# Kernel optimization log

Measured on AMD Instinct MI355X. Metric: run time of the kernel, lower is better.

Reference implementation:

```python
import jax, jax.numpy as jnp
import numpy as np

D = 2048
N = 16384
E = 8
THRESHOLD = 0.5


def setup_inputs() -> dict:
    key = jax.random.key(0)
    ks = jax.random.split(key, 6)
    x = jax.random.normal(ks[0], (N, D), dtype=jnp.float32)
    # pretrained weight + truncated SVD basis (frozen in original module)
    W_np = np.asarray(jax.random.normal(ks[1], (D, D), dtype=jnp.float32))
    U, S, Vt = np.linalg.svd(W_np, full_matrices=False)
    k = int((np.cumsum(S) < THRESHOLD * S.sum()).sum())  # energy-threshold rank
    U_k = jnp.asarray(U[:, :k])
    V_k = jnp.asarray(Vt.T[:, :k])  # torch.svd returns V, not V^T
    W = jnp.asarray(W_np)
    lambda_k = jax.random.normal(ks[2], (E, k), dtype=jnp.float32)
    v = jnp.zeros((D,), dtype=jnp.float32)
    W_g1 = jax.random.normal(ks[3], (k, 1), dtype=jnp.float32)
    W_g2 = jax.random.normal(ks[4], (1, E), dtype=jnp.float32)
    return {"x": x, "W": W, "U_k": U_k, "V_k": V_k, "lambda_k": lambda_k,
            "v": v, "W_g1": W_g1, "W_g2": W_g2}


def reference(x, W, U_k, V_k, lambda_k, v, W_g1, W_g2):
    # Routing: g = softmax((x @ U_k) @ W_g1 @ W_g2)  -> [N, E]
    xu = x @ U_k                                   # [N, k] (shared with delta path)
    g = jax.nn.softmax((xu @ W_g1) @ W_g2, axis=-1)
    # sum_i g_i * (x @ (W + U diag(lam_i) V^T))
    #   = (x@W) * sum_i g_i  +  ((x@U) * (g @ lam)) @ V^T   (low-rank factored)
    base = x @ W                                   # [N, D], computed once
    coef = g @ lambda_k                            # [N, k]
    out = base * jnp.sum(g, axis=-1, keepdims=True) + (xu * coef) @ V_k.T
    return out * (1.0 + v)
```

## Files before the change

kernel.cpp:

```cpp
#include <hip/hip_runtime.h>
#include <hip/hip_bf16.h>

#define D_DIM 2048
#define E_DIM 8

typedef __attribute__((ext_vector_type(8))) short short8;
typedef __attribute__((ext_vector_type(4))) float f32x4;

__device__ __forceinline__ unsigned short f2bf(float f) {
  union { float f; unsigned int u; } v; v.f = f;
  unsigned int u = v.u;
  u += 0x7FFFu + ((u >> 16) & 1u);
  return (unsigned short)(u >> 16);
}

__device__ __forceinline__ float bf2f(unsigned short h) {
  union { unsigned int u; float f; } v; v.u = ((unsigned int)h) << 16;
  return v.f;
}

__device__ __forceinline__ void async_copy16(const void* g, void* l) {
  __builtin_amdgcn_global_load_lds((const __attribute__((address_space(1))) void*)g,
                                   (__attribute__((address_space(3))) void*)l,
                                   16, 0, 0);
}

__global__ void k_cvt_bf16(const float* __restrict__ in,
                           unsigned short* __restrict__ out, long long n) {
  long long i = ((long long)blockIdx.x * blockDim.x + threadIdx.x) * 8;
  const long long stride = (long long)gridDim.x * blockDim.x * 8;
  for (; i < n; i += stride) {
    float4 a = *(const float4*)(in + i);
    float4 b = *(const float4*)(in + i + 4);
    short8 r;
    r[0] = (short)f2bf(a.x); r[1] = (short)f2bf(a.y);
    r[2] = (short)f2bf(a.z); r[3] = (short)f2bf(a.w);
    r[4] = (short)f2bf(b.x); r[5] = (short)f2bf(b.y);
    r[6] = (short)f2bf(b.z); r[7] = (short)f2bf(b.w);
    *(short8*)(out + i) = r;
  }
}

__global__ void k_transpose_bf16(const float* __restrict__ in, int in_rows, int in_cols,
                                 int in_ld, unsigned short* __restrict__ out, int out_rows) {
  __shared__ float tile[32][33];
  const int tx = threadIdx.x;
  const int ty = threadIdx.y;
  const int c = blockIdx.x * 32 + tx;
  #pragma unroll
  for (int i = 0; i < 4; ++i) {
    const int r = blockIdx.y * 32 + ty + i * 8;
    float vv = 0.0f;
    if (r < in_rows && c < in_cols) vv = in[(size_t)r * in_ld + c];
    tile[ty + i * 8][tx] = vv;
  }
  __syncthreads();
  const int oc = blockIdx.y * 32 + tx;
  #pragma unroll
  for (int i = 0; i < 4; ++i) {
    const int orow = blockIdx.x * 32 + ty + i * 8;
    if (orow < out_rows && oc < in_rows)
      out[(size_t)orow * in_rows + oc] = f2bf(tile[tx][ty + i * 8]);
  }
}

__global__ void k_pad_bf16(const float* __restrict__ in, unsigned short* __restrict__ out,
                           int rows, int cols, int cols_pad) {
  long long idx = (long long)blockIdx.x * blockDim.x + threadIdx.x;
  const long long total = (long long)rows * cols_pad;
  const long long stride = (long long)gridDim.x * blockDim.x;
  for (; idx < total; idx += stride) {
    const int r = (int)(idx / cols_pad);
    const int c = (int)(idx % cols_pad);
    out[idx] = (c < cols) ? f2bf(in[(size_t)r * cols + c]) : (unsigned short)0;
  }
}

__global__ void k_u1(const float* __restrict__ U, const float* __restrict__ Wg1,
                     float* __restrict__ u1, int D, int k) {
  const int w = threadIdx.x >> 6;
  const int lane = threadIdx.x & 63;
  const int d = blockIdx.x * 4 + w;
  if (d >= D) return;
  const float* row = U + (size_t)d * k;
  float s = 0.0f;
  for (int j = lane; j < k; j += 64) s += row[j] * Wg1[j];
  #pragma unroll
  for (int off = 32; off; off >>= 1) s += __shfl_xor(s, off);
  if (lane == 0) u1[d] = s;
}

__global__ void k_gate(const unsigned short* __restrict__ xb,
                       const float* __restrict__ u1, const float* __restrict__ Wg2,
                       float* __restrict__ g8, int Nrows) {
  const int w = threadIdx.x >> 6;
  const int lane = threadIdx.x & 63;
  const int row = blockIdx.x * 4 + w;
  if (row >= Nrows) return;
  const unsigned short* xr = xb + (size_t)row * D_DIM;
  float s = 0.0f;
  #pragma unroll
  for (int t = 0; t < D_DIM / 512; ++t) {
    const int base = (t * 64 + lane) * 8;
    short8 v = *(const short8*)(xr + base);
    float4 ua = *(const float4*)(u1 + base);
    float4 ub = *(const float4*)(u1 + base + 4);
    s += bf2f((unsigned short)v[0]) * ua.x + bf2f((unsigned short)v[1]) * ua.y +
         bf2f((unsigned short)v[2]) * ua.z + bf2f((unsigned short)v[3]) * ua.w +
         bf2f((unsigned short)v[4]) * ub.x + bf2f((unsigned short)v[5]) * ub.y +
         bf2f((unsigned short)v[6]) * ub.z + bf2f((unsigned short)v[7]) * ub.w;
  }
  #pragma unroll
  for (int off = 32; off; off >>= 1) s += __shfl_xor(s, off);
  if (lane == 0) {
    float lg[E_DIM], mx = -INFINITY;
    #pragma unroll
    for (int e = 0; e < E_DIM; ++e) { lg[e] = s * Wg2[e]; mx = fmaxf(mx, lg[e]); }
    float Z = 0.0f;
    #pragma unroll
    for (int e = 0; e < E_DIM; ++e) { lg[e] = expf(lg[e] - mx); Z += lg[e]; }
    const float inv = 1.0f / Z;
    #pragma unroll
    for (int e = 0; e < E_DIM; ++e) g8[(size_t)row * E_DIM + e] = lg[e] * inv;
  }
}

__global__ __launch_bounds__(256, 3) void k_gemm128(
    const unsigned short* __restrict__ A, long long lda,
    const unsigned short* __restrict__ B, long long ldb,
    int Ktot,
    const float* __restrict__ g8, const float* __restrict__ lam, int k_real,
    unsigned short* __restrict__ A2, int lda2) {
  __shared__ unsigned short lds[2 * 8192];
  const int tid = threadIdx.x;
  const int lane = tid & 63;
  const int w = tid >> 6;
  const long long brow = (long long)blockIdx.x * 128;
  const long long bcol = (long long)blockIdx.y * 128;
  const int c0 = w * 2;
  const int sr0 = lane >> 2;
  const int sj  = lane & 3;
  const int l15 = lane & 15;
  const int jhi = lane >> 4;
  const int wr = (w >> 1) * 64;
  const int wc = (w & 1) * 64;

  auto stage = [&](int tt) {
    unsigned short* dstA = lds + (tt & 1) * 8192;
    #pragma unroll
    for (int c = 0; c < 2; ++c) {
      const int chunk = c0 + c;
      const int lrow = chunk * 16 + sr0;
      const int jj = sj ^ ((lrow >> 1) & 3);
      async_copy16(A + (brow + lrow) * lda + (long long)tt * 32 + jj * 8,
                   (void*)(dstA + chunk * 512));
      async_copy16(B + (bcol + lrow) * ldb + (long long)tt * 32 + jj * 8,
                   (void*)(dstA + 4096 + chunk * 512));
    }
  };

  f32x4 acc[4][4];
  #pragma unroll
  for (int m = 0; m < 4; ++m)
    #pragma unroll
    for (int n = 0; n < 4; ++n)
      #pragma unroll
      for (int j = 0; j < 4; ++j) acc[m][n][j] = 0.0f;

  const int NT = Ktot >> 5;
  stage(0);
  asm volatile("s_waitcnt vmcnt(0)" ::: "memory");
  __builtin_amdgcn_s_barrier();

  for (int t = 0; t < NT; ++t) {
    const unsigned short* Areg = lds + (t & 1) * 8192;
    const unsigned short* Breg = Areg + 4096;
    if (t + 1 < NT) stage(t + 1);
    short8 av[4], bv[4];
    #pragma unroll
    for (int m = 0; m < 4; ++m) {
      const int row = wr + m * 16 + l15;
      const int jj = jhi ^ ((row >> 1) & 3);
      av[m] = *(const short8*)(Areg + row * 32 + jj * 8);
    }
    #pragma unroll
    for (int n = 0; n < 4; ++n) {
      const int row = wc + n * 16 + l15;
      const int jj = jhi ^ ((row >> 1) & 3);
      bv[n] = *(const short8*)(Breg + row * 32 + jj * 8);
    }
    __builtin_amdgcn_s_setprio(1);
    #pragma unroll
    for (int m = 0; m < 4; ++m)
      #pragma unroll
      for (int n = 0; n < 4; ++n)
        acc[m][n] = __builtin_amdgcn_mfma_f32_16x16x32_bf16(av[m], bv[n], acc[m][n], 0, 0, 0);
    __builtin_amdgcn_s_setprio(0);
    asm volatile("s_waitcnt vmcnt(0)" ::: "memory");
    __builtin_amdgcn_s_barrier();
  }

  float lamE[E_DIM][4];
  #pragma unroll
  for (int n = 0; n < 4; ++n) {
    const long long col = bcol + wc + n * 16 + l15;
    #pragma unroll
    for (int e = 0; e < E_DIM; ++e)
      lamE[e][n] = (col < k_real) ? lam[(size_t)e * k_real + col] : 0.0f;
  }
  #pragma unroll
  for (int m = 0; m < 4; ++m) {
    float coef[4][4];
    #pragma unroll
    for (int j = 0; j < 4; ++j)
      #pragma unroll
      for (int n = 0; n < 4; ++n) coef[j][n] = 0.0f;
    #pragma unroll
    for (int j = 0; j < 4; ++j) {
      const long long row = brow + wr + m * 16 + jhi * 4 + j;
      const float* gr = g8 + row * E_DIM;
      #pragma unroll
      for (int e = 0; e < E_DIM; ++e) {
        const float ge = gr[e];
        #pragma unroll
        for (int n = 0; n < 4; ++n) coef[j][n] += ge * lamE[e][n];
      }
    }
    #pragma unroll
    for (int n = 0; n < 4; ++n) {
      const long long col = bcol + wc + n * 16 + l15;
      #pragma unroll
      for (int j = 0; j < 4; ++j) {
        const long long row = brow + wr + m * 16 + jhi * 4 + j;
        A2[row * lda2 + col] = f2bf(acc[m][n][j] * coef[j][n]);
      }
    }
  }
}

template<int EPI>
__global__ __launch_bounds__(512, 2) void k_gemm256(
    const unsigned short* __restrict__ A0, int lda0,
    const unsigned short* __restrict__ A1, int lda1,
    const unsigned short* __restrict__ B0, int ldb0,
    const unsigned short* __restrict__ B1, int ldb1,
    int ka0, int Ktot, int gridM,
    float* __restrict__ Cout, int ldc,
    const float* __restrict__ vcol) {
  __shared__ unsigned short lds[4 * 16384];
  const int tid = threadIdx.x;
  const int lane = tid & 63;
  const int w = tid >> 6;
  const int wm = w >> 2;
  const int wn = w & 3;

  int bid = blockIdx.x;
  const int cpx = gridDim.x >> 3;
  bid = (bid & 7) * cpx + (bid >> 3);
  const int bx = bid % gridM;
  const int by = bid / gridM;
  const long long brow = (long long)bx * 256;
  const long long bcol = (long long)by * 256;

  const int c0 = w * 2;
  const int sr0 = lane >> 2;
  const int sj  = lane & 3;
  const int l15 = lane & 15;
  const int jhi = lane >> 4;

  auto stage = [&](int tt) {
    const int k0 = tt * 32;
    const unsigned short* PA; long long ldA; long long kA;
    const unsigned short* PB; long long ldB; long long kB;
    if (k0 < ka0) { PA = A0; ldA = lda0; kA = k0;       PB = B0; ldB = ldb0; kB = k0; }
    else          { PA = A1; ldA = lda1; kA = k0 - ka0; PB = B1; ldB = ldb1; kB = k0 - ka0; }
    unsigned short* dst = lds + (tt & 3) * 16384;
    #pragma unroll
    for (int c = 0; c < 2; ++c) {
      const int chunk = c0 + c;
      const int lrow = chunk * 16 + sr0;
      const int jj = sj ^ ((lrow >> 1) & 3);
      async_copy16(PA + (brow + lrow) * ldA + kA + jj * 8, (void*)(dst + chunk * 512));
      async_copy16(PB + (bcol + lrow) * ldB + kB + jj * 8, (void*)(dst + 8192 + chunk * 512));
    }
  };

  auto load_frags = [&](int tt, short8* av, short8* bv) {
    const unsigned short* Areg = lds + (tt & 3) * 16384;
    const unsigned short* Breg = Areg + 8192;
    #pragma unroll
    for (int m = 0; m < 8; ++m) {
      const int row = wm * 128 + m * 16 + l15;
      const int jj = jhi ^ ((row >> 1) & 3);
      av[m] = *(const short8*)(Areg + row * 32 + jj * 8);
    }
    #pragma unroll
    for (int n = 0; n < 4; ++n) {
      const int row = wn * 64 + n * 16 + l15;
      const int jj = jhi ^ ((row >> 1) & 3);
      bv[n] = *(const short8*)(Breg + row * 32 + jj * 8);
    }
  };

  f32x4 acc[8][4];
  #pragma unroll
  for (int m = 0; m < 8; ++m)
    #pragma unroll
    for (int n = 0; n < 4; ++n)
      #pragma unroll
      for (int j = 0; j < 4; ++j) acc[m][n][j] = 0.0f;

  auto do_mfma = [&](short8* av, short8* bv) {
    __builtin_amdgcn_s_setprio(1);
    #pragma unroll
    for (int m = 0; m < 8; ++m)
      #pragma unroll
      for (int n = 0; n < 4; ++n)
        acc[m][n] = __builtin_amdgcn_mfma_f32_16x16x32_bf16(av[m], bv[n], acc[m][n], 0, 0, 0);
    __builtin_amdgcn_s_setprio(0);
  };

  const int NT = Ktot >> 5;
  stage(0); stage(1); stage(2);
  asm volatile("s_waitcnt vmcnt(4)" ::: "memory");
  __builtin_amdgcn_s_barrier();

  short8 avA[8], bvA[4], avB[8], bvB[4];
  load_frags(0, avA, bvA);

  for (int t = 0; t < NT; t += 2) {
    if (t + 3 < NT) stage(t + 3);
    load_frags(t + 1, avB, bvB);
    do_mfma(avA, bvA);
    asm volatile("s_waitcnt vmcnt(4)" ::: "memory");
    __builtin_amdgcn_s_barrier();
    if (t + 4 < NT) stage(t + 4);
    if (t + 2 < NT) load_frags(t + 2, avA, bvA);
    do_mfma(avB, bvB);
    asm volatile("s_waitcnt vmcnt(4)" ::: "memory");
    __builtin_amdgcn_s_barrier();
  }

  #pragma unroll
  for (int m = 0; m < 8; ++m) {
    #pragma unroll
    for (int n = 0; n < 4; ++n) {
      const long long col = bcol + wn * 64 + n * 16 + l15;
      float cs = 1.0f;
      if (EPI == 1) cs = 1.0f + vcol[col];
      #pragma unroll
      for (int j = 0; j < 4; ++j) {
        const long long row = brow + wm * 128 + m * 16 + jhi * 4 + j;
        Cout[row * ldc + col] = acc[m][n][j] * cs;
      }
    }
  }
}

extern "C" void kernel_launch(void* const* d_in, const int* in_sizes, int n_in,
                              void* d_out, int out_size, void* d_ws, size_t ws_size,
                              hipStream_t stream) {
  const float* x   = (const float*)d_in[0];
  const float* W   = (const float*)d_in[1];
  const float* U   = (const float*)d_in[2];
  const float* V   = (const float*)d_in[3];
  const float* lam = (const float*)d_in[4];
  const float* v   = (const float*)d_in[5];
  const float* Wg1 = (const float*)d_in[6];
  const float* Wg2 = (const float*)d_in[7];
  float* out = (float*)d_out;

  const int N = in_sizes[0] / D_DIM;
  const int k = in_sizes[2] / D_DIM;
  const int k_pad = (k + 127) & ~127;

  char* ws = (char*)d_ws;
  size_t off = 0;
  auto alloc = [&](size_t bytes) -> void* {
    void* p = ws + off;
    off += (bytes + 255) & ~(size_t)255;
    return p;
  };
  unsigned short* xb  = (unsigned short*)alloc((size_t)N * D_DIM * 2);
  unsigned short* Wt  = (unsigned short*)alloc((size_t)D_DIM * D_DIM * 2);
  unsigned short* Ukt = (unsigned short*)alloc((size_t)k_pad * D_DIM * 2);
  unsigned short* Vb  = (unsigned short*)alloc((size_t)D_DIM * k_pad * 2);
  unsigned short* A2  = (unsigned short*)alloc((size_t)N * k_pad * 2);
  float*          u1  = (float*)alloc((size_t)D_DIM * 4);
  float*          g8  = (float*)alloc((size_t)N * E_DIM * 4);
  if (off > ws_size) return;

  k_cvt_bf16<<<2048, 256, 0, stream>>>(x, xb, (long long)N * D_DIM);
  k_transpose_bf16<<<dim3(D_DIM / 32, D_DIM / 32), dim3(32, 8), 0, stream>>>(
      W, D_DIM, D_DIM, D_DIM, Wt, D_DIM);
  k_transpose_bf16<<<dim3(k_pad / 32, D_DIM / 32), dim3(32, 8), 0, stream>>>(
      U, D_DIM, k, k, Ukt, k_pad);
  k_pad_bf16<<<512, 256, 0, stream>>>(V, Vb, D_DIM, k, k_pad);
  k_u1<<<D_DIM / 4, 256, 0, stream>>>(U, Wg1, u1, D_DIM, k);

  k_gate<<<N / 4, 256, 0, stream>>>(xb, u1, Wg2, g8, N);

  k_gemm128<<<dim3(N / 128, k_pad / 128), 256, 0, stream>>>(
      xb, D_DIM, Ukt, D_DIM, D_DIM, g8, lam, k, A2, k_pad);

  const int gridM = N / 256;
  const int gridN = D_DIM / 256;
  k_gemm256<1><<<gridM * gridN, 512, 0, stream>>>(
      xb, D_DIM, A2, k_pad,
      Wt, D_DIM, Vb, k_pad,
      D_DIM, D_DIM + k_pad, gridM,
      out, D_DIM, v);
}
```

Baseline: 327.8 us.

## Fuse x bf16 conversion into gate kernel and switch main GEMM to 32x32 MFMA

Merges the standalone fp32-to-bf16 conversion of x into the gating kernel, so x is read once in fp32 and the gate dot product uses full-precision values while the bf16 copy is written. This drops one full read of the bf16 x buffer and a kernel launch. The large 256-tile GEMM now uses 32x32x16 bf16 MFMA instead of 16x16x32, with fragment loads and the epilogue row mapping rewritten to match. That cuts the number of MFMA issues and LDS fragment reads per tile, but the epilogue store pattern changes.

```diff
diff --git a/kernel.cpp b/kernel.cpp
--- a/kernel.cpp
+++ b/kernel.cpp
@@ -6,6 +6,7 @@
 
 typedef __attribute__((ext_vector_type(8))) short short8;
 typedef __attribute__((ext_vector_type(4))) float f32x4;
+typedef __attribute__((ext_vector_type(16))) float f32x16;
 
 __device__ __forceinline__ unsigned short f2bf(float f) {
   union { float f; unsigned int u; } v; v.f = f;
@@ -14,31 +15,10 @@
   return (unsigned short)(u >> 16);
 }
 
-__device__ __forceinline__ float bf2f(unsigned short h) {
-  union { unsigned int u; float f; } v; v.u = ((unsigned int)h) << 16;
-  return v.f;
-}
-
 __device__ __forceinline__ void async_copy16(const void* g, void* l) {
   __builtin_amdgcn_global_load_lds((const __attribute__((address_space(1))) void*)g,
                                    (__attribute__((address_space(3))) void*)l,
                                    16, 0, 0);
-}
-
-__global__ void k_cvt_bf16(const float* __restrict__ in,
-                           unsigned short* __restrict__ out, long long n) {
-  long long i = ((long long)blockIdx.x * blockDim.x + threadIdx.x) * 8;
-  const long long stride = (long long)gridDim.x * blockDim.x * 8;
-  for (; i < n; i += stride) {
-    float4 a = *(const float4*)(in + i);
-    float4 b = *(const float4*)(in + i + 4);
-    short8 r;
-    r[0] = (short)f2bf(a.x); r[1] = (short)f2bf(a.y);
-    r[2] = (short)f2bf(a.z); r[3] = (short)f2bf(a.w);
-    r[4] = (short)f2bf(b.x); r[5] = (short)f2bf(b.y);
-    r[6] = (short)f2bf(b.z); r[7] = (short)f2bf(b.w);
-    *(short8*)(out + i) = r;
-  }
 }
 
 __global__ void k_transpose_bf16(const float* __restrict__ in, int in_rows, int in_cols,
@@ -90,25 +70,32 @@
   if (lane == 0) u1[d] = s;
 }
 
-__global__ void k_gate(const unsigned short* __restrict__ xb,
-                       const float* __restrict__ u1, const float* __restrict__ Wg2,
-                       float* __restrict__ g8, int Nrows) {
+__global__ void k_cvtgate(const float* __restrict__ x,
+                          unsigned short* __restrict__ xb,
+                          const float* __restrict__ u1, const float* __restrict__ Wg2,
+                          float* __restrict__ g8, int Nrows) {
   const int w = threadIdx.x >> 6;
   const int lane = threadIdx.x & 63;
   const int row = blockIdx.x * 4 + w;
   if (row >= Nrows) return;
-  const unsigned short* xr = xb + (size_t)row * D_DIM;
+  const float* xr = x + (size_t)row * D_DIM;
+  unsigned short* xo = xb + (size_t)row * D_DIM;
   float s = 0.0f;
   #pragma unroll
   for (int t = 0; t < D_DIM / 512; ++t) {
     const int base = (t * 64 + lane) * 8;
-    short8 v = *(const short8*)(xr + base);
+    float4 a = *(const float4*)(xr + base);
+    float4 b = *(const float4*)(xr + base + 4);
     float4 ua = *(const float4*)(u1 + base);
     float4 ub = *(const float4*)(u1 + base + 4);
-    s += bf2f((unsigned short)v[0]) * ua.x + bf2f((unsigned short)v[1]) * ua.y +
-         bf2f((unsigned short)v[2]) * ua.z + bf2f((unsigned short)v[3]) * ua.w +
-         bf2f((unsigned short)v[4]) * ub.x + bf2f((unsigned short)v[5]) * ub.y +
-         bf2f((unsigned short)v[6]) * ub.z + bf2f((unsigned short)v[7]) * ub.w;
+    s += a.x * ua.x + a.y * ua.y + a.z * ua.z + a.w * ua.w +
+         b.x * ub.x + b.y * ub.y + b.z * ub.z + b.w * ub.w;
+    short8 r;
+    r[0] = (short)f2bf(a.x); r[1] = (short)f2bf(a.y);
+    r[2] = (short)f2bf(a.z); r[3] = (short)f2bf(a.w);
+    r[4] = (short)f2bf(b.x); r[5] = (short)f2bf(b.y);
+    r[6] = (short)f2bf(b.z); r[7] = (short)f2bf(b.w);
+    *(short8*)(xo + base) = r;
   }
   #pragma unroll
   for (int off = 32; off; off >>= 1) s += __shfl_xor(s, off);
@@ -265,8 +252,8 @@
   const int c0 = w * 2;
   const int sr0 = lane >> 2;
   const int sj  = lane & 3;
-  const int l15 = lane & 15;
-  const int jhi = lane >> 4;
+  const int r31 = lane & 31;
+  const int khalf = lane >> 5;
 
   auto stage = [&](int tt) {
     const int k0 = tt * 32;
@@ -289,34 +276,45 @@
     const unsigned short* Areg = lds + (tt & 3) * 16384;
     const unsigned short* Breg = Areg + 8192;
     #pragma unroll
-    for (int m = 0; m < 8; ++m) {
-      const int row = wm * 128 + m * 16 + l15;
-      const int jj = jhi ^ ((row >> 1) & 3);
-      av[m] = *(const short8*)(Areg + row * 32 + jj * 8);
-    }
-    #pragma unroll
-    for (int n = 0; n < 4; ++n) {
-      const int row = wn * 64 + n * 16 + l15;
-      const int jj = jhi ^ ((row >> 1) & 3);
-      bv[n] = *(const short8*)(Breg + row * 32 + jj * 8);
+    for (int mm = 0; mm < 4; ++mm) {
+      const int row = wm * 128 + mm * 32 + r31;
+      const int swz = (row >> 1) & 3;
+      #pragma unroll
+      for (int k2 = 0; k2 < 2; ++k2) {
+        const int gs = k2 * 2 + khalf;
+        av[mm * 2 + k2] = *(const short8*)(Areg + row * 32 + (gs ^ swz) * 8);
+      }
+    }
+    #pragma unroll
+    for (int nn = 0; nn < 2; ++nn) {
+      const int row = wn * 64 + nn * 32 + r31;
+      const int swz = (row >> 1) & 3;
+      #pragma unroll
+      for (int k2 = 0; k2 < 2; ++k2) {
+        const int gs = k2 * 2 + khalf;
+        bv[nn * 2 + k2] = *(const short8*)(Breg + row * 32 + (gs ^ swz) * 8);
+      }
     }
   };
 
-  f32x4 acc[8][4];
-  #pragma unroll
-  for (int m = 0; m < 8; ++m)
-    #pragma unroll
-    for (int n = 0; n < 4; ++n)
-      #pragma unroll
-      for (int j = 0; j < 4; ++j) acc[m][n][j] = 0.0f;
+  f32x16 acc[4][2];
+  #pragma unroll
+  for (int mm = 0; mm < 4; ++mm)
+    #pragma unroll
+    for (int nn = 0; nn < 2; ++nn)
+      #pragma unroll
+      for (int q = 0; q < 16; ++q) acc[mm][nn][q] = 0.0f;
 
   auto do_mfma = [&](short8* av, short8* bv) {
     __builtin_amdgcn_s_setprio(1);
     #pragma unroll
-    for (int m = 0; m < 8; ++m)
-      #pragma unroll
-      for (int n = 0; n < 4; ++n)
-        acc[m][n] = __builtin_amdgcn_mfma_f32_16x16x32_bf16(av[m], bv[n], acc[m][n], 0, 0, 0);
+    for (int mm = 0; mm < 4; ++mm)
+      #pragma unroll
+      for (int nn = 0; nn < 2; ++nn)
+        #pragma unroll
+        for (int k2 = 0; k2 < 2; ++k2)
+          acc[mm][nn] = __builtin_amdgcn_mfma_f32_32x32x16_bf16(
+              av[mm * 2 + k2], bv[nn * 2 + k2], acc[mm][nn], 0, 0, 0);
     __builtin_amdgcn_s_setprio(0);
   };
 
@@ -342,16 +340,16 @@
   }
 
   #pragma unroll
-  for (int m = 0; m < 8; ++m) {
-    #pragma unroll
-    for (int n = 0; n < 4; ++n) {
-      const long long col = bcol + wn * 64 + n * 16 + l15;
+  for (int mm = 0; mm < 4; ++mm) {
+    #pragma unroll
+    for (int nn = 0; nn < 2; ++nn) {
+      const long long col = bcol + wn * 64 + nn * 32 + r31;
       float cs = 1.0f;
       if (EPI == 1) cs = 1.0f + vcol[col];
       #pragma unroll
-      for (int j = 0; j < 4; ++j) {
-        const long long row = brow + wm * 128 + m * 16 + jhi * 4 + j;
-        Cout[row * ldc + col] = acc[m][n][j] * cs;
+      for (int q = 0; q < 16; ++q) {
+        const long long row = brow + wm * 128 + mm * 32 + (q & 3) + 8 * (q >> 2) + 4 * khalf;
+        Cout[row * ldc + col] = acc[mm][nn][q] * cs;
       }
     }
   }
@@ -390,15 +388,13 @@
   float*          g8  = (float*)alloc((size_t)N * E_DIM * 4);
   if (off > ws_size) return;
 
-  k_cvt_bf16<<<2048, 256, 0, stream>>>(x, xb, (long long)N * D_DIM);
+  k_u1<<<D_DIM / 4, 256, 0, stream>>>(U, Wg1, u1, D_DIM, k);
+  k_cvtgate<<<N / 4, 256, 0, stream>>>(x, xb, u1, Wg2, g8, N);
   k_transpose_bf16<<<dim3(D_DIM / 32, D_DIM / 32), dim3(32, 8), 0, stream>>>(
       W, D_DIM, D_DIM, D_DIM, Wt, D_DIM);
   k_transpose_bf16<<<dim3(k_pad / 32, D_DIM / 32), dim3(32, 8), 0, stream>>>(
       U, D_DIM, k, k, Ukt, k_pad);
   k_pad_bf16<<<512, 256, 0, stream>>>(V, Vb, D_DIM, k, k_pad);
-  k_u1<<<D_DIM / 4, 256, 0, stream>>>(U, Wg1, u1, D_DIM, k);
-
-  k_gate<<<N / 4, 256, 0, stream>>>(xb, u1, Wg2, g8, N);
 
   k_gemm128<<<dim3(N / 128, k_pad / 128), 256, 0, stream>>>(
       xb, D_DIM, Ukt, D_DIM, D_DIM, g8, lam, k, A2, k_pad);
```

New measurement: 326.6 us. No clear change (-0.4%).
